# Optimization experiments

Hardware: AMD Instinct MI355X
Metric: run time of the kernel (lower is better)

Reference implementation:

```python
import jax, jax.numpy as jnp
import numpy as np

B, T = 8192, 4096

def setup_inputs() -> dict:
    key = jax.random.key(0)
    x = jax.random.randint(key, (B, T, 1), 0, 5).astype(jnp.float32)
    alpha = jnp.full((1, 1), 0.1, dtype=jnp.float32)  # smoothing weight for demand level Z
    beta = jnp.full((1, 1), 0.1, dtype=jnp.float32)   # smoothing weight for demand probability P
    return {"x": x, "alpha": alpha, "beta": beta}


def reference(x, alpha, beta):
    # Faithful translation of the Keras TSBRNN cell stepped over time by RNN().
    # NOTE (faithful to source): the cell unpacks states as (Z, P) but returns
    # them as [P_next, Z_next], so the two states SWAP roles every step.
    # Also faithful: X = inputs[0] uses only the FIRST batch row's value in the
    # level update, while the zero-mask is computed over the full batch.
    batch = x.shape[0]

    def step(carry, x_t):
        Z, P = carry                      # each (B, 1)
        X = x_t[0]                        # (1,) first batch row, as in source
        nz = (x_t != 0).astype(x_t.dtype) # (B, 1) non-zero demand mask
        Z_next = alpha * X + (1.0 - alpha) * Z
        Z_next = Z_next * nz + Z * (1.0 - nz)
        P_next = nz * beta + (1.0 - beta) * P
        out = P_next * Z_next             # TSB forecast = prob * level
        return (P_next, Z_next), out      # swapped order, faithful to source

    Z0 = jnp.zeros((batch, 1), x.dtype)
    P0 = jnp.zeros((batch, 1), x.dtype)
    xs = jnp.swapaxes(x, 0, 1)            # (T, B, 1) time-major for scan
    _, ys = jax.lax.scan(step, (Z0, P0), xs)
    return jnp.swapaxes(ys, 0, 1)         # (B, T, 1) full output sequence
```

## Files before the change

kernel.cpp:

```cpp
#include <hip/hip_runtime.h>


constexpr int T_LEN  = 4096;
constexpr int TILE   = 1024;
constexpr int NTILE  = T_LEN / TILE;
constexpr int CHUNK  = TILE / 64;
constexpr int WPB    = 4;
constexpr int PADREG = TILE + 2 * (TILE / 32);

__global__ __launch_bounds__(256, 6) void tsb_scan_kernel(
    const float* __restrict__ x,
    const float* __restrict__ alpha_p,
    const float* __restrict__ beta_p,
    float* __restrict__ out,
    int B)
{
    __shared__ float lds[WPB * PADREG];

    const int tid  = threadIdx.x;
    const int wave = tid >> 6;
    const int lane = tid & 63;
    int row = blockIdx.x * WPB + wave;
    if (row >= B) row = B - 1;

    float* xl = &lds[wave * PADREG];

    const float a   = alpha_p[0];
    const float b   = beta_p[0];
    const float oma = 1.0f - a;
    const float omb = 1.0f - b;

    const int cb = 16 * lane + 2 * (lane >> 1);

    float C1 = 0.f, C2 = 0.f;

    for (int t = 0; t < NTILE; ++t) {
        const float4* xr4 = (const float4*)(x + (size_t)row * T_LEN + t * TILE);

#pragma unroll
        for (int i = 0; i < 4; ++i) {
            float4 vx = xr4[i * 64 + lane];
            int e0 = i * 256 + 4 * lane;
            int bq = e0 + 2 * (e0 >> 5);
            *(float2*)&xl[bq]     = make_float2(vx.x, vx.y);
            *(float2*)&xl[bq + 2] = make_float2(vx.z, vx.w);
        }

        const float* Xt = x + t * TILE + 16 * lane;

        float p = 1.f, u = 0.f, q = 1.f, v = 0.f;
#pragma unroll
        for (int h = 0; h < CHUNK / 2; ++h) {
            float2 xp = *(const float2*)&xl[cb + 2 * h];
            float2 Xp = *(const float2*)(Xt + 2 * h);
            float x1 = xp.x, x2 = xp.y;
            float nz1 = (x1 != 0.f) ? 1.f : 0.f;
            float nz2 = (x2 != 0.f) ? 1.f : 0.f;
            float k1  = (x1 != 0.f) ? oma : 1.f;
            float k2  = (x2 != 0.f) ? oma : 1.f;
            float P = omb * k1;
            float U = omb * a * nz1 * Xp.x + b * nz2;
            float Q = omb * k2;
            float V = b * k2 * nz1 + a * nz2 * Xp.y;
            u = P * u + U;  p = P * p;
            v = Q * v + V;  q = Q * q;
        }

#pragma unroll
        for (int off = 1; off < 64; off <<= 1) {
            float pi = __shfl_up(p, off, 64);
            float ui = __shfl_up(u, off, 64);
            float qi = __shfl_up(q, off, 64);
            float vi = __shfl_up(v, off, 64);
            if (lane >= off) {
                u = p * ui + u;  p = p * pi;
                v = q * vi + v;  q = q * qi;
            }
        }
        float pp = __shfl_up(p, 1, 64), up = __shfl_up(u, 1, 64);
        float qp = __shfl_up(q, 1, 64), vp = __shfl_up(v, 1, 64);
        float c1 = (lane == 0) ? C1 : (pp * C1 + up);
        float c2 = (lane == 0) ? C2 : (qp * C2 + vp);
        float p63 = __shfl(p, 63, 64), u63 = __shfl(u, 63, 64);
        float q63 = __shfl(q, 63, 64), v63 = __shfl(v, 63, 64);
        float C1n = p63 * C1 + u63;
        float C2n = q63 * C2 + v63;
        C1 = C1n;  C2 = C2n;

#pragma unroll
        for (int h = 0; h < CHUNK / 2; ++h) {
            float2 xp = *(const float2*)&xl[cb + 2 * h];
            float2 Xp = *(const float2*)(Xt + 2 * h);
            bool  nzA = (xp.x != 0.f);
            float c2A = nzA ? (a * Xp.x + oma * c1) : c1;
            float c1A = (nzA ? b : 0.f) + omb * c2;
            bool  nzB = (xp.y != 0.f);
            float c2B = nzB ? (a * Xp.y + oma * c1A) : c1A;
            float c1B = (nzB ? b : 0.f) + omb * c2A;
            c1 = c1B;  c2 = c2B;
            *(float2*)&xl[cb + 2 * h] = make_float2(c1A * c2A, c1B * c2B);
        }

        float4* or4 = (float4*)(out + (size_t)row * T_LEN + t * TILE);
#pragma unroll
        for (int i = 0; i < 4; ++i) {
            int e0 = i * 256 + 4 * lane;
            int bq = e0 + 2 * (e0 >> 5);
            float2 w0 = *(const float2*)&xl[bq];
            float2 w1 = *(const float2*)&xl[bq + 2];
            or4[i * 64 + lane] = make_float4(w0.x, w0.y, w1.x, w1.y);
        }
    }
}

extern "C" void kernel_launch(void* const* d_in, const int* in_sizes, int n_in,
                              void* d_out, int out_size, void* d_ws, size_t ws_size,
                              hipStream_t stream) {
    const float* x     = (const float*)d_in[0];
    const float* alpha = (const float*)d_in[1];
    const float* beta  = (const float*)d_in[2];
    float* out = (float*)d_out;

    const int B = in_sizes[0] / T_LEN;
    const int blocks = (B + WPB - 1) / WPB;
    tsb_scan_kernel<<<blocks, 64 * WPB, 0, stream>>>(x, alpha, beta, out, B);
}
```

Before: 254.2 us.

## Process two rows per wave with smaller time tiles for more ILP

Each wavefront now scans two batch rows at once, interleaving their independent recurrences, and the time tile shrinks from 1024 to 512 so each lane handles 8 steps instead of 16. Interleaving the two rows gives the shuffle-based wave scan twice as much independent work per step and shares the first-row X loads between them, which should hide shuffle latency. The price is more passes over the time axis, roughly twice the scan state in registers, and removal of the occupancy hint from the launch bounds. The row clamping also changes and assumes B is even.

```diff
diff --git a/kernel.cpp b/kernel.cpp
--- a/kernel.cpp
+++ b/kernel.cpp
@@ -1,114 +1,166 @@
 #include <hip/hip_runtime.h>
 
 
-constexpr int T_LEN  = 4096;
-constexpr int TILE   = 1024;
-constexpr int NTILE  = T_LEN / TILE;
-constexpr int CHUNK  = TILE / 64;
-constexpr int WPB    = 4;
-constexpr int PADREG = TILE + 2 * (TILE / 32);
+constexpr int T_LEN = 4096;
+constexpr int TILE  = 512;
+constexpr int NTILE = T_LEN / TILE;
+constexpr int WPB   = 4;
+constexpr int PADT  = TILE + 2 * (TILE / 32);
 
-__global__ __launch_bounds__(256, 6) void tsb_scan_kernel(
+__global__ __launch_bounds__(256) void tsb_scan_kernel(
     const float* __restrict__ x,
     const float* __restrict__ alpha_p,
     const float* __restrict__ beta_p,
     float* __restrict__ out,
     int B)
 {
-    __shared__ float lds[WPB * PADREG];
+    __shared__ float lds[WPB * 2 * PADT];
 
     const int tid  = threadIdx.x;
     const int wave = tid >> 6;
     const int lane = tid & 63;
-    int row = blockIdx.x * WPB + wave;
-    if (row >= B) row = B - 1;
+    int rowA = blockIdx.x * (2 * WPB) + 2 * wave;
+    if (rowA + 1 >= B) rowA = B - 2;
+    const int rowB = rowA + 1;
 
-    float* xl = &lds[wave * PADREG];
+    float* bufA = &lds[wave * 2 * PADT];
+    float* bufB = bufA + PADT;
 
     const float a   = alpha_p[0];
     const float b   = beta_p[0];
     const float oma = 1.0f - a;
     const float omb = 1.0f - b;
 
-    const int cb = 16 * lane + 2 * (lane >> 1);
+    const int cb = 8 * lane + 2 * (lane >> 2);
 
-    float C1 = 0.f, C2 = 0.f;
+    float C1A = 0.f, C2A = 0.f, C1B = 0.f, C2B = 0.f;
+
+    const float* xrA = x + (size_t)rowA * T_LEN;
+    const float* xrB = x + (size_t)rowB * T_LEN;
 
     for (int t = 0; t < NTILE; ++t) {
-        const float4* xr4 = (const float4*)(x + (size_t)row * T_LEN + t * TILE);
+        const float4* a4 = (const float4*)(xrA + t * TILE);
+        const float4* b4 = (const float4*)(xrB + t * TILE);
 
-#pragma unroll
-        for (int i = 0; i < 4; ++i) {
-            float4 vx = xr4[i * 64 + lane];
-            int e0 = i * 256 + 4 * lane;
-            int bq = e0 + 2 * (e0 >> 5);
-            *(float2*)&xl[bq]     = make_float2(vx.x, vx.y);
-            *(float2*)&xl[bq + 2] = make_float2(vx.z, vx.w);
+        float4 va0 = a4[lane], va1 = a4[64 + lane];
+        float4 vb0 = b4[lane], vb1 = b4[64 + lane];
+
+        {
+            int e0 = 4 * lane;        int q0 = e0 + 2 * (e0 >> 5);
+            int e1 = 256 + 4 * lane;  int q1 = e1 + 2 * (e1 >> 5);
+            *(float2*)&bufA[q0]     = make_float2(va0.x, va0.y);
+            *(float2*)&bufA[q0 + 2] = make_float2(va0.z, va0.w);
+            *(float2*)&bufA[q1]     = make_float2(va1.x, va1.y);
+            *(float2*)&bufA[q1 + 2] = make_float2(va1.z, va1.w);
+            *(float2*)&bufB[q0]     = make_float2(vb0.x, vb0.y);
+            *(float2*)&bufB[q0 + 2] = make_float2(vb0.z, vb0.w);
+            *(float2*)&bufB[q1]     = make_float2(vb1.x, vb1.y);
+            *(float2*)&bufB[q1 + 2] = make_float2(vb1.z, vb1.w);
         }
 
-        const float* Xt = x + t * TILE + 16 * lane;
+        const float* Xt = x + t * TILE + 8 * lane;
 
-        float p = 1.f, u = 0.f, q = 1.f, v = 0.f;
+        float pA = 1.f, uA = 0.f, qA = 1.f, vA = 0.f;
+        float pB = 1.f, uB = 0.f, qB = 1.f, vB = 0.f;
 #pragma unroll
-        for (int h = 0; h < CHUNK / 2; ++h) {
-            float2 xp = *(const float2*)&xl[cb + 2 * h];
+        for (int h = 0; h < 4; ++h) {
             float2 Xp = *(const float2*)(Xt + 2 * h);
-            float x1 = xp.x, x2 = xp.y;
-            float nz1 = (x1 != 0.f) ? 1.f : 0.f;
-            float nz2 = (x2 != 0.f) ? 1.f : 0.f;
-            float k1  = (x1 != 0.f) ? oma : 1.f;
-            float k2  = (x2 != 0.f) ? oma : 1.f;
-            float P = omb * k1;
-            float U = omb * a * nz1 * Xp.x + b * nz2;
-            float Q = omb * k2;
-            float V = b * k2 * nz1 + a * nz2 * Xp.y;
-            u = P * u + U;  p = P * p;
-            v = Q * v + V;  q = Q * q;
+            float2 xa = *(const float2*)&bufA[cb + 2 * h];
+            float2 xb = *(const float2*)&bufB[cb + 2 * h];
+            {
+                float nz1 = (xa.x != 0.f) ? 1.f : 0.f;
+                float nz2 = (xa.y != 0.f) ? 1.f : 0.f;
+                float k1  = (xa.x != 0.f) ? oma : 1.f;
+                float k2  = (xa.y != 0.f) ? oma : 1.f;
+                float P = omb * k1;
+                float U = omb * a * nz1 * Xp.x + b * nz2;
+                float Q = omb * k2;
+                float V = b * k2 * nz1 + a * nz2 * Xp.y;
+                uA = P * uA + U;  pA = P * pA;
+                vA = Q * vA + V;  qA = Q * qA;
+            }
+            {
+                float nz1 = (xb.x != 0.f) ? 1.f : 0.f;
+                float nz2 = (xb.y != 0.f) ? 1.f : 0.f;
+                float k1  = (xb.x != 0.f) ? oma : 1.f;
+                float k2  = (xb.y != 0.f) ? oma : 1.f;
+                float P = omb * k1;
+                float U = omb * a * nz1 * Xp.x + b * nz2;
+                float Q = omb * k2;
+                float V = b * k2 * nz1 + a * nz2 * Xp.y;
+                uB = P * uB + U;  pB = P * pB;
+                vB = Q * vB + V;  qB = Q * qB;
+            }
         }
 
 #pragma unroll
         for (int off = 1; off < 64; off <<= 1) {
-            float pi = __shfl_up(p, off, 64);
-            float ui = __shfl_up(u, off, 64);
-            float qi = __shfl_up(q, off, 64);
-            float vi = __shfl_up(v, off, 64);
+            float piA = __shfl_up(pA, off, 64), uiA = __shfl_up(uA, off, 64);
+            float qiA = __shfl_up(qA, off, 64), viA = __shfl_up(vA, off, 64);
+            float piB = __shfl_up(pB, off, 64), uiB = __shfl_up(uB, off, 64);
+            float qiB = __shfl_up(qB, off, 64), viB = __shfl_up(vB, off, 64);
             if (lane >= off) {
-                u = p * ui + u;  p = p * pi;
-                v = q * vi + v;  q = q * qi;
+                uA = pA * uiA + uA;  pA = pA * piA;
+                vA = qA * viA + vA;  qA = qA * qiA;
+                uB = pB * uiB + uB;  pB = pB * piB;
+                vB = qB * viB + vB;  qB = qB * qiB;
             }
         }
-        float pp = __shfl_up(p, 1, 64), up = __shfl_up(u, 1, 64);
-        float qp = __shfl_up(q, 1, 64), vp = __shfl_up(v, 1, 64);
-        float c1 = (lane == 0) ? C1 : (pp * C1 + up);
-        float c2 = (lane == 0) ? C2 : (qp * C2 + vp);
-        float p63 = __shfl(p, 63, 64), u63 = __shfl(u, 63, 64);
-        float q63 = __shfl(q, 63, 64), v63 = __shfl(v, 63, 64);
-        float C1n = p63 * C1 + u63;
-        float C2n = q63 * C2 + v63;
-        C1 = C1n;  C2 = C2n;
+        float ppA = __shfl_up(pA, 1, 64), upA = __shfl_up(uA, 1, 64);
+        float qpA = __shfl_up(qA, 1, 64), vpA = __shfl_up(vA, 1, 64);
+        float ppB = __shfl_up(pB, 1, 64), upB = __shfl_up(uB, 1, 64);
+        float qpB = __shfl_up(qB, 1, 64), vpB = __shfl_up(vB, 1, 64);
+        float c1A = (lane == 0) ? C1A : (ppA * C1A + upA);
+        float c2A = (lane == 0) ? C2A : (qpA * C2A + vpA);
+        float c1B = (lane == 0) ? C1B : (ppB * C1B + upB);
+        float c2B = (lane == 0) ? C2B : (qpB * C2B + vpB);
+        float p63A = __shfl(pA, 63, 64), u63A = __shfl(uA, 63, 64);
+        float q63A = __shfl(qA, 63, 64), v63A = __shfl(vA, 63, 64);
+        float p63B = __shfl(pB, 63, 64), u63B = __shfl(uB, 63, 64);
+        float q63B = __shfl(qB, 63, 64), v63B = __shfl(vB, 63, 64);
+        float nC1A = p63A * C1A + u63A, nC2A = q63A * C2A + v63A;
+        float nC1B = p63B * C1B + u63B, nC2B = q63B * C2B + v63B;
+        C1A = nC1A;  C2A = nC2A;  C1B = nC1B;  C2B = nC2B;
 
 #pragma unroll
-        for (int h = 0; h < CHUNK / 2; ++h) {
-            float2 xp = *(const float2*)&xl[cb + 2 * h];
+        for (int h = 0; h < 4; ++h) {
             float2 Xp = *(const float2*)(Xt + 2 * h);
-            bool  nzA = (xp.x != 0.f);
-            float c2A = nzA ? (a * Xp.x + oma * c1) : c1;
-            float c1A = (nzA ? b : 0.f) + omb * c2;
-            bool  nzB = (xp.y != 0.f);
-            float c2B = nzB ? (a * Xp.y + oma * c1A) : c1A;
-            float c1B = (nzB ? b : 0.f) + omb * c2A;
-            c1 = c1B;  c2 = c2B;
-            *(float2*)&xl[cb + 2 * h] = make_float2(c1A * c2A, c1B * c2B);
+            float2 xa = *(const float2*)&bufA[cb + 2 * h];
+            float2 xb = *(const float2*)&bufB[cb + 2 * h];
+            {
+                bool  nz1 = (xa.x != 0.f);
+                float c2n = nz1 ? (a * Xp.x + oma * c1A) : c1A;
+                float c1n = (nz1 ? b : 0.f) + omb * c2A;
+                bool  nz2 = (xa.y != 0.f);
+                float c2m = nz2 ? (a * Xp.y + oma * c1n) : c1n;
+                float c1m = (nz2 ? b : 0.f) + omb * c2n;
+                c1A = c1m;  c2A = c2m;
+                *(float2*)&bufA[cb + 2 * h] = make_float2(c1n * c2n, c1m * c2m);
+            }
+            {
+                bool  nz1 = (xb.x != 0.f);
+                float c2n = nz1 ? (a * Xp.x + oma * c1B) : c1B;
+                float c1n = (nz1 ? b : 0.f) + omb * c2B;
+                bool  nz2 = (xb.y != 0.f);
+                float c2m = nz2 ? (a * Xp.y + oma * c1n) : c1n;
+                float c1m = (nz2 ? b : 0.f) + omb * c2n;
+                c1B = c1m;  c2B = c2m;
+                *(float2*)&bufB[cb + 2 * h] = make_float2(c1n * c2n, c1m * c2m);
+            }
         }
 
-        float4* or4 = (float4*)(out + (size_t)row * T_LEN + t * TILE);
+        float4* oA = (float4*)(out + (size_t)rowA * T_LEN + t * TILE);
+        float4* oB = (float4*)(out + (size_t)rowB * T_LEN + t * TILE);
 #pragma unroll
-        for (int i = 0; i < 4; ++i) {
+        for (int i = 0; i < 2; ++i) {
             int e0 = i * 256 + 4 * lane;
-            int bq = e0 + 2 * (e0 >> 5);
-            float2 w0 = *(const float2*)&xl[bq];
-            float2 w1 = *(const float2*)&xl[bq + 2];
-            or4[i * 64 + lane] = make_float4(w0.x, w0.y, w1.x, w1.y);
+            int qq = e0 + 2 * (e0 >> 5);
+            float2 wa0 = *(const float2*)&bufA[qq];
+            float2 wa1 = *(const float2*)&bufA[qq + 2];
+            float2 wb0 = *(const float2*)&bufB[qq];
+            float2 wb1 = *(const float2*)&bufB[qq + 2];
+            oA[i * 64 + lane] = make_float4(wa0.x, wa0.y, wa1.x, wa1.y);
+            oB[i * 64 + lane] = make_float4(wb0.x, wb0.y, wb1.x, wb1.y);
         }
     }
 }
@@ -122,6 +174,7 @@
     float* out = (float*)d_out;
 
     const int B = in_sizes[0] / T_LEN;
-    const int blocks = (B + WPB - 1) / WPB;
+    const int rows_per_block = 2 * WPB;
+    const int blocks = (B + rows_per_block - 1) / rows_per_block;
     tsb_scan_kernel<<<blocks, 64 * WPB, 0, stream>>>(x, alpha, beta, out, B);
 }
```

After: 243.9 us. 1.04x faster.
